# Performance work log

Hardware: AMD Instinct MI355X
Metric: run time of the kernel (lower is better)

The kernel has to match this reference:

```python
import jax, jax.numpy as jnp
import numpy as np

B, L, E, H = 128, 256, 256, 512


def setup_inputs() -> dict:
    key = jax.random.key(0)
    ks = jax.random.split(key, 16)
    s = 0.02
    return {
        "embedded_inputs": jax.random.normal(ks[0], (B, L, E), jnp.float32),
        "decoder_input": jax.random.normal(ks[1], (B, E), jnp.float32),
        "dec_h": jax.random.normal(ks[2], (B, H), jnp.float32),
        "dec_c": jax.random.normal(ks[3], (B, H), jnp.float32),
        "context": jax.random.normal(ks[4], (B, L, H), jnp.float32),
        # Decoder params
        "W_i2h": jax.random.normal(ks[5], (4 * H, E), jnp.float32) * s,
        "b_i2h": jnp.zeros((4 * H,), jnp.float32),
        "W_h2h": jax.random.normal(ks[6], (4 * H, H), jnp.float32) * s,
        "b_h2h": jnp.zeros((4 * H,), jnp.float32),
        "W_out": jax.random.normal(ks[7], (H, 2 * H), jnp.float32) * s,
        "b_out": jnp.zeros((H,), jnp.float32),
        # Attention params
        "W_inp": jax.random.normal(ks[8], (H, H), jnp.float32) * s,
        "b_inp": jnp.zeros((H,), jnp.float32),
        "W_ctx": jax.random.normal(ks[9], (H, H), jnp.float32) * s,  # Conv1d(k=1) kernel squeezed
        "b_ctx": jnp.zeros((H,), jnp.float32),
        "V": jax.random.uniform(ks[10], (H,), jnp.float32, -1.0, 1.0),
    }


def reference(embedded_inputs, decoder_input, dec_h, dec_c, context,
              W_i2h, b_i2h, W_h2h, b_h2h, W_out, b_out,
              W_inp, b_inp, W_ctx, b_ctx, V):
    # Precompute projected context: Conv1d(k=1) == per-position linear. ctx: [B, H, L]
    ctx = jnp.einsum("blh,gh->bgl", context, W_ctx) + b_ctx[None, :, None]
    seq_len = embedded_inputs.shape[1]

    def step(carry, _):
        x, h, c, mask = carry
        gates = x @ W_i2h.T + b_i2h + h @ W_h2h.T + b_h2h
        i, f, g, o = jnp.split(gates, 4, axis=1)
        c_t = jax.nn.sigmoid(f) * c + jax.nn.sigmoid(i) * jnp.tanh(g)
        h_t = jax.nn.sigmoid(o) * jnp.tanh(c_t)
        # attention
        inp = h_t @ W_inp.T + b_inp                              # [B, H]
        scores = jnp.einsum("h,bhl->bl", V, jnp.tanh(inp[:, :, None] + ctx))
        att = jnp.where(mask == 0, -jnp.inf, scores)
        alpha = jax.nn.softmax(att, axis=-1)                     # [B, L]
        hidden = jnp.einsum("bhl,bl->bh", ctx, alpha)
        h_new = jnp.tanh(jnp.concatenate([hidden, h_t], axis=1) @ W_out.T + b_out)
        # pointer selection
        idx = jnp.argmax(alpha * mask, axis=1)                   # [B]
        one_hot = jax.nn.one_hot(idx, seq_len, dtype=mask.dtype)
        mask_new = mask * (1.0 - one_hot)
        next_x = jnp.take_along_axis(embedded_inputs, idx[:, None, None], axis=1)[:, 0, :]
        return (next_x, h_new, c_t, mask_new), (alpha, idx)

    mask0 = jnp.ones((embedded_inputs.shape[0], seq_len), jnp.float32)
    (x_f, h_f, c_f, _), (alphas, ptrs) = jax.lax.scan(
        step, (decoder_input, dec_h, dec_c, mask0), None, length=seq_len)
    outputs = jnp.transpose(alphas, (1, 0, 2))   # [B, L, L]
    pointers = jnp.transpose(ptrs, (1, 0))       # [B, L]
    return outputs, pointers, h_f, c_f
```

## Files before the change

kernel.cpp:

```cpp
#include <hip/hip_runtime.h>

#define B 128
#define L 256
#define E 256
#define H 512
#define NBLK 256
#define NTHR 512

typedef float f4 __attribute__((ext_vector_type(4)));

#define WS_CTX 0u
#define WS_HT  18874368u
#define WS_HH  18939904u
#define WS_HID 19005440u
#define WS_INP 19071232u
#define WS_XT  19136768u
#define WS_FLG 19169536u

#define OUT_ALPHA 0u
#define OUT_PTR   8388608u
#define OUT_H     8421376u
#define OUT_C     8486912u

#define L2E 1.4426950408889634f

__device__ __forceinline__ float fast_rcp(float x) { return __builtin_amdgcn_rcpf(x); }

__device__ __forceinline__ float ftanh(float x) {
  float e = exp2f(x * (2.0f * L2E));
  return 1.0f - 2.0f * fast_rcp(e + 1.0f);
}
__device__ __forceinline__ float fsig(float x) {
  float e = exp2f(-x * L2E);
  return fast_rcp(1.0f + e);
}

#define CLD1(v0, p0)                                                          \
  asm volatile("global_load_dwordx4 %0, %1, off sc0 sc1\n\t"                  \
               "s_waitcnt vmcnt(0)"                                           \
               : "=&v"(v0) : "v"(p0) : "memory")

#define CLD2(va, pa)                                                          \
  asm volatile("global_load_dwordx4 %0, %2, off sc0 sc1\n\t"                  \
               "global_load_dwordx4 %1, %3, off sc0 sc1\n\t"                  \
               "s_waitcnt vmcnt(0)"                                           \
               : "=&v"(va[0]), "=&v"(va[1])                                   \
               : "v"(pa[0]), "v"(pa[1]) : "memory")

#define CLD4(va, pa)                                                          \
  asm volatile("global_load_dwordx4 %0, %4, off sc0 sc1\n\t"                  \
               "global_load_dwordx4 %1, %5, off sc0 sc1\n\t"                  \
               "global_load_dwordx4 %2, %6, off sc0 sc1\n\t"                  \
               "global_load_dwordx4 %3, %7, off sc0 sc1\n\t"                  \
               "s_waitcnt vmcnt(0)"                                           \
               : "=&v"(va[0]), "=&v"(va[1]), "=&v"(va[2]), "=&v"(va[3])       \
               : "v"(pa[0]), "v"(pa[1]), "v"(pa[2]), "v"(pa[3]) : "memory")

#define CLD6(va, pa)                                                          \
  asm volatile("global_load_dwordx4 %0, %6, off sc0 sc1\n\t"                  \
               "global_load_dwordx4 %1, %7, off sc0 sc1\n\t"                  \
               "global_load_dwordx4 %2, %8, off sc0 sc1\n\t"                  \
               "global_load_dwordx4 %3, %9, off sc0 sc1\n\t"                  \
               "global_load_dwordx4 %4, %10, off sc0 sc1\n\t"                 \
               "global_load_dwordx4 %5, %11, off sc0 sc1\n\t"                 \
               "s_waitcnt vmcnt(0)"                                           \
               : "=&v"(va[0]), "=&v"(va[1]), "=&v"(va[2]), "=&v"(va[3]),      \
                 "=&v"(va[4]), "=&v"(va[5])                                   \
               : "v"(pa[0]), "v"(pa[1]), "v"(pa[2]), "v"(pa[3]),              \
                 "v"(pa[4]), "v"(pa[5]) : "memory")

#define CST4_1(p0, v0)                                                        \
  asm volatile("global_store_dwordx4 %0, %1, off sc0 sc1\n\t"                 \
               "s_waitcnt expcnt(0)"                                          \
               :: "v"(p0), "v"(v0) : "memory")

__device__ __forceinline__ void gbar(unsigned* flags, unsigned tgt) {
  asm volatile("s_waitcnt vmcnt(0) lgkmcnt(0) expcnt(0)" ::: "memory");
  __syncthreads();
  if (threadIdx.x == 0) {
    unsigned* p = flags + blockIdx.x * 16;
    asm volatile("global_store_dword %0, %1, off sc0 sc1" :: "v"(p), "v"(tgt) : "memory");
  }
  if (blockIdx.x == 0) {
    if (threadIdx.x < 64) {
      const unsigned* p0 = flags + (threadIdx.x * 4 + 0) * 16;
      const unsigned* p1 = flags + (threadIdx.x * 4 + 1) * 16;
      const unsigned* p2 = flags + (threadIdx.x * 4 + 2) * 16;
      const unsigned* p3 = flags + (threadIdx.x * 4 + 3) * 16;
      for (;;) {
        unsigned f0, f1, f2, f3;
        asm volatile("global_load_dword %0, %4, off sc0 sc1\n\t"
                     "global_load_dword %1, %5, off sc0 sc1\n\t"
                     "global_load_dword %2, %6, off sc0 sc1\n\t"
                     "global_load_dword %3, %7, off sc0 sc1\n\t"
                     "s_waitcnt vmcnt(0)"
                     : "=&v"(f0), "=&v"(f1), "=&v"(f2), "=&v"(f3)
                     : "v"(p0), "v"(p1), "v"(p2), "v"(p3) : "memory");
        if (__all(f0 >= tgt && f1 >= tgt && f2 >= tgt && f3 >= tgt)) break;
        __builtin_amdgcn_s_sleep(1);
      }
    }
    __syncthreads();
    if (threadIdx.x < 8) {
      unsigned* gp = flags + 4096 + threadIdx.x * 16;
      asm volatile("global_store_dword %0, %1, off sc0 sc1" :: "v"(gp), "v"(tgt) : "memory");
    }
  } else {
    if (threadIdx.x == 0) {
      const unsigned* gp = flags + 4096 + (blockIdx.x & 7) * 16;
      for (;;) {
        unsigned g;
        asm volatile("global_load_dword %0, %1, off sc0 sc1\n\ts_waitcnt vmcnt(0)"
                     : "=&v"(g) : "v"(gp) : "memory");
        if (g >= tgt) break;
        __builtin_amdgcn_s_sleep(2);
      }
    }
  }
  __syncthreads();
}

__global__ __launch_bounds__(256) void k_ctx(const float* __restrict__ context,
                                             const float* __restrict__ Wc,
                                             const float* __restrict__ bc,
                                             float* __restrict__ ws) {
  __shared__ float a_lds[64][33];
  __shared__ float b_lds[32][68];
  int t = threadIdx.x;
  int m0 = blockIdx.x * 64;
  int n0 = blockIdx.y * 64;
  int tx = t & 15, ty = t >> 4;
  float acc[4][4] = {};
  for (int kc = 0; kc < 16; ++kc) {
    int k0 = kc * 32;
    __syncthreads();
#pragma unroll
    for (int i = 0; i < 2; ++i) {
      int f40 = t + i * 256;
      int mm = f40 >> 3;
      int k4 = (f40 & 7) * 4;
      float4 v = *(const float4*)&context[(size_t)(m0 + mm) * H + k0 + k4];
      a_lds[mm][k4] = v.x; a_lds[mm][k4 + 1] = v.y; a_lds[mm][k4 + 2] = v.z; a_lds[mm][k4 + 3] = v.w;
    }
#pragma unroll
    for (int i = 0; i < 2; ++i) {
      int f40 = t + i * 256;
      int nn = f40 >> 3;
      int k4 = (f40 & 7) * 4;
      float4 v = *(const float4*)&Wc[(size_t)(n0 + nn) * H + k0 + k4];
      b_lds[k4][nn] = v.x; b_lds[k4 + 1][nn] = v.y; b_lds[k4 + 2][nn] = v.z; b_lds[k4 + 3][nn] = v.w;
    }
    __syncthreads();
#pragma unroll
    for (int kk = 0; kk < 32; ++kk) {
      float4 bv = *(const float4*)&b_lds[kk][tx * 4];
      float a0 = a_lds[ty * 4 + 0][kk], a1 = a_lds[ty * 4 + 1][kk];
      float a2 = a_lds[ty * 4 + 2][kk], a3 = a_lds[ty * 4 + 3][kk];
      acc[0][0] += a0 * bv.x; acc[0][1] += a0 * bv.y; acc[0][2] += a0 * bv.z; acc[0][3] += a0 * bv.w;
      acc[1][0] += a1 * bv.x; acc[1][1] += a1 * bv.y; acc[1][2] += a1 * bv.z; acc[1][3] += a1 * bv.w;
      acc[2][0] += a2 * bv.x; acc[2][1] += a2 * bv.y; acc[2][2] += a2 * bv.z; acc[2][3] += a2 * bv.w;
      acc[3][0] += a3 * bv.x; acc[3][1] += a3 * bv.y; acc[3][2] += a3 * bv.z; acc[3][3] += a3 * bv.w;
    }
  }
  float b0v = bc[n0 + tx * 4], b1v = bc[n0 + tx * 4 + 1], b2v = bc[n0 + tx * 4 + 2], b3v = bc[n0 + tx * 4 + 3];
#pragma unroll
  for (int i = 0; i < 4; ++i) {
    size_t o = WS_CTX + (size_t)(m0 + ty * 4 + i) * H + n0 + tx * 4;
    float4 v; v.x = acc[i][0] + b0v; v.y = acc[i][1] + b1v; v.z = acc[i][2] + b2v; v.w = acc[i][3] + b3v;
    *(float4*)&ws[o] = v;
  }
}

__global__ __launch_bounds__(256) void k_init(const float* __restrict__ dec_h,
                                              const float* __restrict__ dec_in,
                                              float* __restrict__ ws) {
  int flat = blockIdx.x * 256 + threadIdx.x;
  if (flat < 65536) {
    ws[WS_HH + flat] = dec_h[flat];
  } else if (flat < 98304) {
    ws[WS_XT + (flat - 65536)] = dec_in[flat - 65536];
  } else if (flat < 102528) {
    ((unsigned*)(ws + WS_FLG))[flat - 98304] = 0u;
  }
}

__global__ __launch_bounds__(512, 1) void k_main(
    const float* __restrict__ Wi2h, const float* __restrict__ bi2h,
    const float* __restrict__ Wh2h, const float* __restrict__ bh2h,
    const float* __restrict__ Wout, const float* __restrict__ bout,
    const float* __restrict__ Winp, const float* __restrict__ binp,
    const float* __restrict__ Vv,   const float* __restrict__ emb,
    const float* __restrict__ dec_c,
    float* __restrict__ ws,         float* __restrict__ out) {
  __shared__ float s_act[13504];
  __shared__ float s_maskP[256];
  __shared__ float s_mw[8], s_dw[8];
  __shared__ float s_red[4];
  __shared__ int   s_redi[4];
  __shared__ int   s_wc[4], s_wb[4];
  __shared__ int   s_mi, s_cnt;

  unsigned* flags = (unsigned*)(ws + WS_FLG);
  const int bid = blockIdx.x;
  const int t = threadIdx.x;
  const int wv = t >> 6, ln = t & 63;
  unsigned tgt = 0;

  float creg = 0.f;

  if (bid < 128 && t < 256) s_maskP[t] = 1.0f;
  __syncthreads();

  for (int step = 0; step < L; ++step) {
    {
      const int jt = (bid & 7) * 4 + ((bid >> 3) & 3);
      const int bt = bid >> 5;
      const int u0 = jt * 16, b0 = bt * 16;
      float* sact = s_act;
      float* sg   = s_act + 12352;
      f4 va[6]; const float* pa[6]; int sb[6], sq[6];
#pragma unroll
      for (int it = 0; it < 6; ++it) {
        unsigned c = (unsigned)(t + it * 512);
        int bl = (int)(c / 192u);
        int kq = (int)(c - (unsigned)bl * 192u);
        int kg = kq * 4;
        sb[it] = bl; sq[it] = kq;
        pa[it] = (kg < 256) ? ws + WS_XT + (size_t)(b0 + bl) * 256 + kg
                            : ws + WS_HH + (size_t)(b0 + bl) * 512 + (kg - 256);
      }
      CLD6(va, pa);
      __builtin_amdgcn_sched_barrier(0);
#pragma unroll
      for (int it = 0; it < 6; ++it) *(f4*)&sact[sb[it] * 772 + sq[it] * 4] = va[it];
      __syncthreads();

      const int jj = t >> 4, bb = t & 15;
      const int g = jj >> 3, up = (jj & 7) * 2;
      const int r0 = g * 512 + u0 + up;
      float a0 = 0.f, a1 = 0.f;
      {
        const float* w0 = Wi2h + (size_t)r0 * 256;
        const float* w1 = w0 + 256;
        const float* sa = sact + bb * 772;
#pragma unroll 8
        for (int k4 = 0; k4 < 64; ++k4) {
          float4 x = *(const float4*)&sa[k4 * 4];
          float4 p = *(const float4*)&w0[k4 * 4];
          float4 q = *(const float4*)&w1[k4 * 4];
          a0 += p.x * x.x + p.y * x.y + p.z * x.z + p.w * x.w;
          a1 += q.x * x.x + q.y * x.y + q.z * x.z + q.w * x.w;
        }
        const float* v0 = Wh2h + (size_t)r0 * 512;
        const float* v1 = v0 + 512;
        const float* shh = sa + 256;
#pragma unroll 8
        for (int k4 = 0; k4 < 128; ++k4) {
          float4 x = *(const float4*)&shh[k4 * 4];
          float4 p = *(const float4*)&v0[k4 * 4];
          float4 q = *(const float4*)&v1[k4 * 4];
          a0 += p.x * x.x + p.y * x.y + p.z * x.z + p.w * x.w;
          a1 += q.x * x.x + q.y * x.y + q.z * x.z + q.w * x.w;
        }
      }
      sg[(g * 16 + up) * 17 + bb]     = a0;
      sg[(g * 16 + up + 1) * 17 + bb] = a1;
      __syncthreads();
      if (t < 256) {
        const int uu = t >> 4, b2 = t & 15;
        const int j0 = u0 + uu;
        float si_ = sg[(     uu) * 17 + b2] + bi2h[       j0] + bh2h[       j0];
        float sf_ = sg[(16 + uu) * 17 + b2] + bi2h[ 512 + j0] + bh2h[ 512 + j0];
        float sg_ = sg[(32 + uu) * 17 + b2] + bi2h[1024 + j0] + bh2h[1024 + j0];
        float so_ = sg[(48 + uu) * 17 + b2] + bi2h[1536 + j0] + bh2h[1536 + j0];
        if (step == 0) creg = dec_c[(size_t)(b0 + b2) * 512 + j0];
        float cn = fsig(sf_) * creg + fsig(si_) * ftanh(sg_);
        creg = cn;
        float htv = fsig(so_) * ftanh(cn);
        s_act[b2 * 17 + uu] = htv;
        if (step == L - 1) out[OUT_C + (size_t)(b0 + b2) * 512 + j0] = cn;
      }
      __syncthreads();
      if (t < 64) {
        const int b2 = t >> 2, q = t & 3;
        f4 hv;
        hv[0] = s_act[b2 * 17 + q * 4 + 0];
        hv[1] = s_act[b2 * 17 + q * 4 + 1];
        hv[2] = s_act[b2 * 17 + q * 4 + 2];
        hv[3] = s_act[b2 * 17 + q * 4 + 3];
        float* hp = ws + WS_HT + (size_t)(b0 + b2) * 512 + u0 + q * 4;
        CST4_1(hp, hv);
      }
    }
    ++tgt; gbar(flags, tgt);

    {
      const int gt = (bid & 7) * 2 + ((bid >> 3) & 1);
      const int bt = bid >> 4;
      const int g0 = gt * 32, b0 = bt * 8;
      float* si = s_act;
      float* stmp = s_act + 4128;
      f4 va[2]; const float* pa[2];
#pragma unroll
      for (int it = 0; it < 2; ++it) {
        int c = t + it * 512;
        int bl = c >> 7, kq = c & 127;
        pa[it] = ws + WS_HT + (size_t)(b0 + bl) * 512 + kq * 4;
      }
      CLD2(va, pa);
      __builtin_amdgcn_sched_barrier(0);
#pragma unroll
      for (int it = 0; it < 2; ++it) {
        int c = t + it * 512;
        int bl = c >> 7, kq = c & 127;
        *(f4*)&si[bl * 516 + kq * 4] = va[it];
      }
      __syncthreads();
      if (t < 256) {
        const int gl = t >> 3, bb = t & 7;
        const float* w = Winp + (size_t)(g0 + gl) * 512;
        const float* sa = si + bb * 516;
        float acc = 0.f;
#pragma unroll 8
        for (int k4 = 0; k4 < 128; ++k4) {
          float4 ww = *(const float4*)&w[k4 * 4];
          float4 xx = *(const float4*)&sa[k4 * 4];
          acc += ww.x * xx.x + ww.y * xx.y + ww.z * xx.z + ww.w * xx.w;
        }
        stmp[bb * 33 + gl] = acc + binp[g0 + gl];
      }
      __syncthreads();
      if (t < 64) {
        const int bb = t >> 3, q = t & 7;
        f4 v;
        v[0] = stmp[bb * 33 + q * 4 + 0];
        v[1] = stmp[bb * 33 + q * 4 + 1];
        v[2] = stmp[bb * 33 + q * 4 + 2];
        v[3] = stmp[bb * 33 + q * 4 + 3];
        float* p = ws + WS_INP + (size_t)(b0 + bb) * 512 + g0 + q * 4;
        CST4_1(p, v);
      }
    }
    ++tgt; gbar(flags, tgt);

    if (bid < 128) {
      const int b = bid;
      float* s_inp  = s_act;
      float* s_sc   = s_act + 512;
      int*   s_li   = (int*)(s_act + 768);
      float* s_hidp = s_act + 1024;
      float* s_out  = s_act + 5120;
      if (t < 128) {
        f4 v;
        const float* p = ws + WS_INP + (size_t)b * 512 + t * 4;
        CLD1(v, p);
        *(f4*)&s_inp[t * 4] = v;
      }
      __syncthreads();
      const int d0 = ln * 8;
      float inp8[8], v8[8];
#pragma unroll
      for (int i = 0; i < 8; ++i) { inp8[i] = s_inp[d0 + i]; v8[i] = Vv[d0 + i]; }
      bool validl = (t < 256) && (s_maskP[t] != 0.f);
      unsigned long long bal = __ballot(validl);
      if (t < 256 && (t & 63) == 0) s_wc[t >> 6] = (int)__popcll(bal);
      __syncthreads();
      if (t == 0) {
        int base = 0;
#pragma unroll
        for (int i = 0; i < 4; ++i) { s_wb[i] = base; base += s_wc[i]; }
        s_cnt = base;
      }
      __syncthreads();
      if (validl) {
        int idx = s_wb[t >> 6] + (int)__popcll(bal & ((1ull << (t & 63)) - 1ull));
        s_li[idx] = t;
      }
      __syncthreads();
      const int cnt = s_cnt;
      float m = -INFINITY, den = 0.f;
      float hid[8] = {0, 0, 0, 0, 0, 0, 0, 0};
      {
        f4 cur0a, cur0b, cur1a, cur1b, cur2a, cur2b, cur3a, cur3b;
        int l0i, l1i, l2i, l3i;
        int base = wv * 4;
        {
          int s0 = base, s1 = base + 1, s2 = base + 2, s3 = base + 3;
          int a = (s0 < cnt) ? s_li[s0] : 0;  l0i = (s0 < cnt) ? a : -1;
          int bb2 = (s1 < cnt) ? s_li[s1] : 0; l1i = (s1 < cnt) ? bb2 : -1;
          int c = (s2 < cnt) ? s_li[s2] : 0;  l2i = (s2 < cnt) ? c : -1;
          int d = (s3 < cnt) ? s_li[s3] : 0;  l3i = (s3 < cnt) ? d : -1;
          const f4* p0 = (const f4*)(ws + WS_CTX + ((size_t)(b * 256 + a) * 512) + d0);
          const f4* p1 = (const f4*)(ws + WS_CTX + ((size_t)(b * 256 + bb2) * 512) + d0);
          const f4* p2 = (const f4*)(ws + WS_CTX + ((size_t)(b * 256 + c) * 512) + d0);
          const f4* p3 = (const f4*)(ws + WS_CTX + ((size_t)(b * 256 + d) * 512) + d0);
          cur0a = __builtin_nontemporal_load(p0); cur0b = __builtin_nontemporal_load(p0 + 1);
          cur1a = __builtin_nontemporal_load(p1); cur1b = __builtin_nontemporal_load(p1 + 1);
          cur2a = __builtin_nontemporal_load(p2); cur2b = __builtin_nontemporal_load(p2 + 1);
          cur3a = __builtin_nontemporal_load(p3); cur3b = __builtin_nontemporal_load(p3 + 1);
        }
        for (; base < cnt; base += 32) {
          f4 n0a, n0b, n1a, n1b, n2a, n2b, n3a, n3b;
          int nl0, nl1, nl2, nl3;
          {
            int s0 = base + 32, s1 = base + 33, s2 = base + 34, s3 = base + 35;
            int a = (s0 < cnt) ? s_li[s0] : 0;  nl0 = (s0 < cnt) ? a : -1;
            int bb2 = (s1 < cnt) ? s_li[s1] : 0; nl1 = (s1 < cnt) ? bb2 : -1;
            int c = (s2 < cnt) ? s_li[s2] : 0;  nl2 = (s2 < cnt) ? c : -1;
            int d = (s3 < cnt) ? s_li[s3] : 0;  nl3 = (s3 < cnt) ? d : -1;
            const f4* p0 = (const f4*)(ws + WS_CTX + ((size_t)(b * 256 + a) * 512) + d0);
            const f4* p1 = (const f4*)(ws + WS_CTX + ((size_t)(b * 256 + bb2) * 512) + d0);
            const f4* p2 = (const f4*)(ws + WS_CTX + ((size_t)(b * 256 + c) * 512) + d0);
            const f4* p3 = (const f4*)(ws + WS_CTX + ((size_t)(b * 256 + d) * 512) + d0);
            n0a = __builtin_nontemporal_load(p0); n0b = __builtin_nontemporal_load(p0 + 1);
            n1a = __builtin_nontemporal_load(p1); n1b = __builtin_nontemporal_load(p1 + 1);
            n2a = __builtin_nontemporal_load(p2); n2b = __builtin_nontemporal_load(p2 + 1);
            n3a = __builtin_nontemporal_load(p3); n3b = __builtin_nontemporal_load(p3 + 1);
          }
          float sv0, sv1, sv2, sv3;
          {
            float part = v8[0] * ftanh(inp8[0] + cur0a[0]) + v8[1] * ftanh(inp8[1] + cur0a[1])
                       + v8[2] * ftanh(inp8[2] + cur0a[2]) + v8[3] * ftanh(inp8[3] + cur0a[3])
                       + v8[4] * ftanh(inp8[4] + cur0b[0]) + v8[5] * ftanh(inp8[5] + cur0b[1])
                       + v8[6] * ftanh(inp8[6] + cur0b[2]) + v8[7] * ftanh(inp8[7] + cur0b[3]);
#pragma unroll
            for (int off = 32; off > 0; off >>= 1) part += __shfl_xor(part, off);
            if (l0i >= 0 && ln == 0) s_sc[l0i] = part;
            sv0 = (l0i >= 0) ? part : -INFINITY;
          }
          {
            float part = v8[0] * ftanh(inp8[0] + cur1a[0]) + v8[1] * ftanh(inp8[1] + cur1a[1])
                       + v8[2] * ftanh(inp8[2] + cur1a[2]) + v8[3] * ftanh(inp8[3] + cur1a[3])
                       + v8[4] * ftanh(inp8[4] + cur1b[0]) + v8[5] * ftanh(inp8[5] + cur1b[1])
                       + v8[6] * ftanh(inp8[6] + cur1b[2]) + v8[7] * ftanh(inp8[7] + cur1b[3]);
#pragma unroll
            for (int off = 32; off > 0; off >>= 1) part += __shfl_xor(part, off);
            if (l1i >= 0 && ln == 0) s_sc[l1i] = part;
            sv1 = (l1i >= 0) ? part : -INFINITY;
          }
          {
            float part = v8[0] * ftanh(inp8[0] + cur2a[0]) + v8[1] * ftanh(inp8[1] + cur2a[1])
                       + v8[2] * ftanh(inp8[2] + cur2a[2]) + v8[3] * ftanh(inp8[3] + cur2a[3])
                       + v8[4] * ftanh(inp8[4] + cur2b[0]) + v8[5] * ftanh(inp8[5] + cur2b[1])
                       + v8[6] * ftanh(inp8[6] + cur2b[2]) + v8[7] * ftanh(inp8[7] + cur2b[3]);
#pragma unroll
            for (int off = 32; off > 0; off >>= 1) part += __shfl_xor(part, off);
            if (l2i >= 0 && ln == 0) s_sc[l2i] = part;
            sv2 = (l2i >= 0) ? part : -INFINITY;
          }
          {
            float part = v8[0] * ftanh(inp8[0] + cur3a[0]) + v8[1] * ftanh(inp8[1] + cur3a[1])
                       + v8[2] * ftanh(inp8[2] + cur3a[2]) + v8[3] * ftanh(inp8[3] + cur3a[3])
                       + v8[4] * ftanh(inp8[4] + cur3b[0]) + v8[5] * ftanh(inp8[5] + cur3b[1])
                       + v8[6] * ftanh(inp8[6] + cur3b[2]) + v8[7] * ftanh(inp8[7] + cur3b[3]);
#pragma unroll
            for (int off = 32; off > 0; off >>= 1) part += __shfl_xor(part, off);
            if (l3i >= 0 && ln == 0) s_sc[l3i] = part;
            sv3 = (l3i >= 0) ? part : -INFINITY;
          }
          float mn = fmaxf(m, fmaxf(fmaxf(sv0, sv1), fmaxf(sv2, sv3)));
          float scale = exp2f((m - mn) * L2E);
          float e0 = exp2f((sv0 - mn) * L2E);
          float e1 = exp2f((sv1 - mn) * L2E);
          float e2 = exp2f((sv2 - mn) * L2E);
          float e3 = exp2f((sv3 - mn) * L2E);
          den = den * scale + ((e0 + e1) + (e2 + e3));
          hid[0] = hid[0] * scale + e0 * cur0a[0] + e1 * cur1a[0] + e2 * cur2a[0] + e3 * cur3a[0];
          hid[1] = hid[1] * scale + e0 * cur0a[1] + e1 * cur1a[1] + e2 * cur2a[1] + e3 * cur3a[1];
          hid[2] = hid[2] * scale + e0 * cur0a[2] + e1 * cur1a[2] + e2 * cur2a[2] + e3 * cur3a[2];
          hid[3] = hid[3] * scale + e0 * cur0a[3] + e1 * cur1a[3] + e2 * cur2a[3] + e3 * cur3a[3];
          hid[4] = hid[4] * scale + e0 * cur0b[0] + e1 * cur1b[0] + e2 * cur2b[0] + e3 * cur3b[0];
          hid[5] = hid[5] * scale + e0 * cur0b[1] + e1 * cur1b[1] + e2 * cur2b[1] + e3 * cur3b[1];
          hid[6] = hid[6] * scale + e0 * cur0b[2] + e1 * cur1b[2] + e2 * cur2b[2] + e3 * cur3b[2];
          hid[7] = hid[7] * scale + e0 * cur0b[3] + e1 * cur1b[3] + e2 * cur2b[3] + e3 * cur3b[3];
          m = mn;
          cur0a = n0a; cur0b = n0b; cur1a = n1a; cur1b = n1b;
          cur2a = n2a; cur2b = n2b; cur3a = n3a; cur3b = n3b;
          l0i = nl0; l1i = nl1; l2i = nl2; l3i = nl3;
        }
      }
      if (ln == 0) { s_mw[wv] = m; s_dw[wv] = den; }
      __syncthreads();
      float M = s_mw[0];
#pragma unroll
      for (int w = 1; w < 8; ++w) M = fmaxf(M, s_mw[w]);
      float D = 0.f;
#pragma unroll
      for (int w = 0; w < 8; ++w) D += s_dw[w] * exp2f((s_mw[w] - M) * L2E);
      float fac = exp2f((m - M) * L2E);
#pragma unroll
      for (int i = 0; i < 8; ++i) s_hidp[wv * 512 + d0 + i] = hid[i] * fac;
      __syncthreads();
      const float rD = 1.0f / D;
      {
        float hs = 0.f;
#pragma unroll
        for (int w = 0; w < 8; ++w) hs += s_hidp[w * 512 + t];
        s_out[t] = hs * rD;
      }
      float sc = 0.f; bool valid = false;
      if (t < 256) {
        valid = (s_maskP[t] != 0.f);
        sc = s_sc[t];
        float alpha = valid ? exp2f((sc - M) * L2E) * rD : 0.f;
        out[OUT_ALPHA + ((size_t)b * 256 + step) * 256 + t] = alpha;
        float bs = valid ? sc : -INFINITY;
        int bi = t;
#pragma unroll
        for (int off = 32; off > 0; off >>= 1) {
          float os = __shfl_down(bs, off);
          int oi = __shfl_down(bi, off);
          if (os > bs || (os == bs && oi < bi)) { bs = os; bi = oi; }
        }
        if ((t & 63) == 0) { s_red[t >> 6] = bs; s_redi[t >> 6] = bi; }
      }
      __syncthreads();
      if (t == 0) {
        float mm = s_red[0]; int mi = s_redi[0];
#pragma unroll
        for (int w = 1; w < 4; ++w) {
          if (s_red[w] > mm || (s_red[w] == mm && s_redi[w] < mi)) { mm = s_red[w]; mi = s_redi[w]; }
        }
        s_mi = mi;
      }
      __syncthreads();
      const int mi = s_mi;
      if (t < 128) {
        f4 hv = *(const f4*)&s_out[t * 4];
        float* hp = ws + WS_HID + (size_t)b * 512 + t * 4;
        CST4_1(hp, hv);
      }
      if (t < 64) {
        float4 xv = *(const float4*)&emb[((size_t)b * 256 + mi) * 256 + t * 4];
        f4 xq; xq[0] = xv.x; xq[1] = xv.y; xq[2] = xv.z; xq[3] = xv.w;
        float* xp = ws + WS_XT + (size_t)b * 256 + t * 4;
        CST4_1(xp, xq);
      }
      if (t == 0) {
        out[OUT_PTR + (size_t)b * 256 + step] = (float)mi;
        s_maskP[mi] = 0.f;
      }
    }
    ++tgt; gbar(flags, tgt);

    {
      const int rt = (bid & 7) * 2 + ((bid >> 3) & 1);
      const int bt = bid >> 4;
      const int r0 = rt * 32, b0 = bt * 8;
      float* sh = s_act;
      float* stmp = s_act + 8224;
      f4 va[4]; const float* pa[4];
#pragma unroll
      for (int it = 0; it < 4; ++it) {
        int c = t + it * 512;
        int bl = c >> 8, kq = c & 255;
        int kg = kq * 4;
        pa[it] = (kg < 512) ? ws + WS_HID + (size_t)(b0 + bl) * 512 + kg
                            : ws + WS_HT + (size_t)(b0 + bl) * 512 + (kg - 512);
      }
      CLD4(va, pa);
      __builtin_amdgcn_sched_barrier(0);
#pragma unroll
      for (int it = 0; it < 4; ++it) {
        int c = t + it * 512;
        int bl = c >> 8, kq = c & 255;
        *(f4*)&sh[bl * 1028 + kq * 4] = va[it];
      }
      __syncthreads();
      if (t < 256) {
        const int rl = t >> 3, bb = t & 7;
        const float* w = Wout + (size_t)(r0 + rl) * 1024;
        const float* sa = sh + bb * 1028;
        float acc = 0.f;
#pragma unroll 8
        for (int k4 = 0; k4 < 256; ++k4) {
          float4 ww = *(const float4*)&w[k4 * 4];
          float4 xx = *(const float4*)&sa[k4 * 4];
          acc += ww.x * xx.x + ww.y * xx.y + ww.z * xx.z + ww.w * xx.w;
        }
        float h = ftanh(acc + bout[r0 + rl]);
        stmp[bb * 33 + rl] = h;
        if (step == L - 1) out[OUT_H + (size_t)(b0 + bb) * 512 + r0 + rl] = h;
      }
      __syncthreads();
      if (t < 64) {
        const int bb = t >> 3, q = t & 7;
        f4 v;
        v[0] = stmp[bb * 33 + q * 4 + 0];
        v[1] = stmp[bb * 33 + q * 4 + 1];
        v[2] = stmp[bb * 33 + q * 4 + 2];
        v[3] = stmp[bb * 33 + q * 4 + 3];
        float* p = ws + WS_HH + (size_t)(b0 + bb) * 512 + r0 + q * 4;
        CST4_1(p, v);
      }
    }
    ++tgt; gbar(flags, tgt);
  }
}

extern "C" void kernel_launch(void* const* d_in, const int* in_sizes, int n_in,
                              void* d_out, int out_size, void* d_ws, size_t ws_size,
                              hipStream_t stream) {
  (void)in_sizes; (void)n_in; (void)out_size; (void)ws_size;
  const float* emb    = (const float*)d_in[0];
  const float* dec_in = (const float*)d_in[1];
  const float* dec_h  = (const float*)d_in[2];
  const float* dec_c  = (const float*)d_in[3];
  const float* ctx_in = (const float*)d_in[4];
  const float* W_i2h  = (const float*)d_in[5];
  const float* b_i2h  = (const float*)d_in[6];
  const float* W_h2h  = (const float*)d_in[7];
  const float* b_h2h  = (const float*)d_in[8];
  const float* W_out  = (const float*)d_in[9];
  const float* b_out  = (const float*)d_in[10];
  const float* W_inp  = (const float*)d_in[11];
  const float* b_inp  = (const float*)d_in[12];
  const float* W_ctx  = (const float*)d_in[13];
  const float* b_ctx  = (const float*)d_in[14];
  const float* Vv     = (const float*)d_in[15];
  float* out = (float*)d_out;
  float* ws  = (float*)d_ws;

  k_ctx<<<dim3(512, 8), 256, 0, stream>>>(ctx_in, W_ctx, b_ctx, ws);
  k_init<<<401, 256, 0, stream>>>(dec_h, dec_in, ws);
  k_main<<<NBLK, NTHR, 0, stream>>>(W_i2h, b_i2h, W_h2h, b_h2h, W_out, b_out,
                                    W_inp, b_inp, Vv, emb, dec_c, ws, out);
}
```

Before: 16.53 ms.

## Fuse attention input projection into attention phase, removing a grid barrier

Drops the separate distributed W_inp projection phase and its grid-wide barrier. Each attention block (one per batch row) now loads h_t for its own row and computes the full 512-wide projection locally, one output per thread. This removes one global sync and a workspace round trip per step. In exchange each of 128 blocks reads the whole W_inp matrix from cache per step instead of splitting that work across 256 blocks.

```diff
diff --git a/kernel.cpp b/kernel.cpp
--- a/kernel.cpp
+++ b/kernel.cpp
@@ -13,7 +13,6 @@
 #define WS_HT  18874368u
 #define WS_HH  18939904u
 #define WS_HID 19005440u
-#define WS_INP 19071232u
 #define WS_XT  19136768u
 #define WS_FLG 19169536u
 
@@ -39,13 +38,6 @@
   asm volatile("global_load_dwordx4 %0, %1, off sc0 sc1\n\t"                  \
                "s_waitcnt vmcnt(0)"                                           \
                : "=&v"(v0) : "v"(p0) : "memory")
-
-#define CLD2(va, pa)                                                          \
-  asm volatile("global_load_dwordx4 %0, %2, off sc0 sc1\n\t"                  \
-               "global_load_dwordx4 %1, %3, off sc0 sc1\n\t"                  \
-               "s_waitcnt vmcnt(0)"                                           \
-               : "=&v"(va[0]), "=&v"(va[1])                                   \
-               : "v"(pa[0]), "v"(pa[1]) : "memory")
 
 #define CLD4(va, pa)                                                          \
   asm volatile("global_load_dwordx4 %0, %4, off sc0 sc1\n\t"                  \
@@ -234,7 +226,6 @@
 #pragma unroll
       for (int it = 0; it < 6; ++it) *(f4*)&sact[sb[it] * 772 + sq[it] * 4] = va[it];
       __syncthreads();
-
       const int jj = t >> 4, bb = t & 15;
       const int g = jj >> 3, up = (jj & 7) * 2;
       const int r0 = g * 512 + u0 + up;
@@ -294,55 +285,6 @@
     }
     ++tgt; gbar(flags, tgt);
 
-    {
-      const int gt = (bid & 7) * 2 + ((bid >> 3) & 1);
-      const int bt = bid >> 4;
-      const int g0 = gt * 32, b0 = bt * 8;
-      float* si = s_act;
-      float* stmp = s_act + 4128;
-      f4 va[2]; const float* pa[2];
-#pragma unroll
-      for (int it = 0; it < 2; ++it) {
-        int c = t + it * 512;
-        int bl = c >> 7, kq = c & 127;
-        pa[it] = ws + WS_HT + (size_t)(b0 + bl) * 512 + kq * 4;
-      }
-      CLD2(va, pa);
-      __builtin_amdgcn_sched_barrier(0);
-#pragma unroll
-      for (int it = 0; it < 2; ++it) {
-        int c = t + it * 512;
-        int bl = c >> 7, kq = c & 127;
-        *(f4*)&si[bl * 516 + kq * 4] = va[it];
-      }
-      __syncthreads();
-      if (t < 256) {
-        const int gl = t >> 3, bb = t & 7;
-        const float* w = Winp + (size_t)(g0 + gl) * 512;
-        const float* sa = si + bb * 516;
-        float acc = 0.f;
-#pragma unroll 8
-        for (int k4 = 0; k4 < 128; ++k4) {
-          float4 ww = *(const float4*)&w[k4 * 4];
-          float4 xx = *(const float4*)&sa[k4 * 4];
-          acc += ww.x * xx.x + ww.y * xx.y + ww.z * xx.z + ww.w * xx.w;
-        }
-        stmp[bb * 33 + gl] = acc + binp[g0 + gl];
-      }
-      __syncthreads();
-      if (t < 64) {
-        const int bb = t >> 3, q = t & 7;
-        f4 v;
-        v[0] = stmp[bb * 33 + q * 4 + 0];
-        v[1] = stmp[bb * 33 + q * 4 + 1];
-        v[2] = stmp[bb * 33 + q * 4 + 2];
-        v[3] = stmp[bb * 33 + q * 4 + 3];
-        float* p = ws + WS_INP + (size_t)(b0 + bb) * 512 + g0 + q * 4;
-        CST4_1(p, v);
-      }
-    }
-    ++tgt; gbar(flags, tgt);
-
     if (bid < 128) {
       const int b = bid;
       float* s_inp  = s_act;
@@ -350,17 +292,25 @@
       int*   s_li   = (int*)(s_act + 768);
       float* s_hidp = s_act + 1024;
       float* s_out  = s_act + 5120;
+      float* s_ht   = s_act + 5632;
       if (t < 128) {
         f4 v;
-        const float* p = ws + WS_INP + (size_t)b * 512 + t * 4;
+        const float* p = ws + WS_HT + (size_t)b * 512 + t * 4;
         CLD1(v, p);
-        *(f4*)&s_inp[t * 4] = v;
-      }
-      __syncthreads();
-      const int d0 = ln * 8;
-      float inp8[8], v8[8];
-#pragma unroll
-      for (int i = 0; i < 8; ++i) { inp8[i] = s_inp[d0 + i]; v8[i] = Vv[d0 + i]; }
+        *(f4*)&s_ht[t * 4] = v;
+      }
+      __syncthreads();
+      {
+        const float* w = Winp + (size_t)t * 512;
+        float acc = 0.f;
+#pragma unroll 8
+        for (int k4 = 0; k4 < 128; ++k4) {
+          float4 ww = *(const float4*)&w[k4 * 4];
+          float4 xx = *(const float4*)&s_ht[k4 * 4];
+          acc += ww.x * xx.x + ww.y * xx.y + ww.z * xx.z + ww.w * xx.w;
+        }
+        s_inp[t] = acc + binp[t];
+      }
       bool validl = (t < 256) && (s_maskP[t] != 0.f);
       unsigned long long bal = __ballot(validl);
       if (t < 256 && (t & 63) == 0) s_wc[t >> 6] = (int)__popcll(bal);
@@ -378,6 +328,10 @@
       }
       __syncthreads();
       const int cnt = s_cnt;
+      const int d0 = ln * 8;
+      float inp8[8], v8[8];
+#pragma unroll
+      for (int i = 0; i < 8; ++i) { inp8[i] = s_inp[d0 + i]; v8[i] = Vv[d0 + i]; }
       float m = -INFINITY, den = 0.f;
       float hid[8] = {0, 0, 0, 0, 0, 0, 0, 0};
       {
```

After: 22.64 ms. 1.37x slower.
